# Kernel optimization log

Measured on AMD Instinct MI355X. Metric: run time of the kernel, lower is better.

## Reference

```python
import jax, jax.numpy as jnp
import numpy as np

N_NODES = 50000
N_EDGES = 800000
D_IN, D_HID, D_OUT = 128, 128, 64
BN_EPS = 1e-5


def gcn_conv(x, W, b, src, dst, ew, n):
    # PyG GCNConv: out[i] = sum_j norm_ij * (x @ W)[j] + b, with self-loops added
    xw = x @ W                                   # [N, D_out]
    loop = jnp.arange(n)
    s = jnp.concatenate([src, loop])             # add self-loops (weight 1)
    d = jnp.concatenate([dst, loop])
    w = jnp.concatenate([ew, jnp.ones((n,), x.dtype)])
    deg = jax.ops.segment_sum(w, d, num_segments=n)
    dinv = jnp.where(deg > 0, jax.lax.rsqrt(deg), 0.0)
    norm = dinv[s] * w * dinv[d]                 # symmetric normalization
    msg = xw[s] * norm[:, None]                  # gather + scale  [E+N, D_out]
    return jax.ops.segment_sum(msg, d, num_segments=n) + b


def setup_inputs() -> dict:
    key = jax.random.key(0)
    ks = jax.random.split(key, 12)
    x = jax.random.normal(ks[0], (N_NODES, D_IN), dtype=jnp.float32)
    edge_index = jax.random.randint(ks[1], (2, N_EDGES), 0, N_NODES, dtype=jnp.int64)
    edge_weight = jax.random.uniform(ks[2], (N_EDGES,), dtype=jnp.float32)
    W1 = jax.random.normal(ks[3], (D_IN, D_HID), dtype=jnp.float32) * 0.05
    b1 = jnp.zeros((D_HID,), jnp.float32)
    gamma = jnp.ones((D_HID,), jnp.float32)
    beta = jnp.zeros((D_HID,), jnp.float32)
    running_mean = jax.random.normal(ks[4], (D_HID,), dtype=jnp.float32) * 0.1
    running_var = jax.random.uniform(ks[5], (D_HID,), dtype=jnp.float32) + 0.5
    W2 = jax.random.normal(ks[6], (D_HID, D_OUT), dtype=jnp.float32) * 0.05
    b2 = jnp.zeros((D_OUT,), jnp.float32)
    return {"x": x, "edge_index": edge_index, "edge_weight": edge_weight,
            "W1": W1, "b1": b1, "gamma": gamma, "beta": beta,
            "running_mean": running_mean, "running_var": running_var,
            "W2": W2, "b2": b2}


def reference(x, edge_index, edge_weight, W1, b1, gamma, beta,
              running_mean, running_var, W2, b2):
    src, dst = edge_index[0], edge_index[1]
    n = x.shape[0]
    h = gcn_conv(x, W1, b1, src, dst, edge_weight, n)
    # BatchNorm1d in eval mode (running stats); dropout inactive in eval
    h = (h - running_mean) * jax.lax.rsqrt(running_var + BN_EPS) * gamma + beta
    h = jax.nn.relu(h)
    out = gcn_conv(h, W2, b2, src, dst, edge_weight, n)
    return out
```

## Files before the change

### kernel.cpp

```cpp
#include <hip/hip_runtime.h>
#include <hip/hip_fp16.h>

#define BN_EPS 1e-5f
#define PAD 64

static __device__ __forceinline__ unsigned short f2bf(float f) {
    unsigned u = __float_as_uint(f);
    u += 0x7FFF + ((u >> 16) & 1);
    return (unsigned short)(u >> 16);
}
static __device__ __forceinline__ float bf2f(unsigned short b) {
    return __uint_as_float((unsigned)b << 16);
}
static __device__ __forceinline__ unsigned pk(int s, float w) {
    return ((unsigned)s << 16) | (unsigned)__half_as_ushort(__float2half_rn(w));
}
static __device__ __forceinline__ float pw(unsigned e) {
    return __half2float(__ushort_as_half((unsigned short)(e & 0xFFFFu)));
}

__global__ __launch_bounds__(256) void k_fused(const int* __restrict__ src, const int* __restrict__ dst,
                                               const float* __restrict__ ew,
                                               int* cnt, unsigned* __restrict__ pad, int e, int gfill, int stride,
                                               const float* __restrict__ A, const float* __restrict__ W,
                                               unsigned short* __restrict__ C, int n,
                                               const float* __restrict__ b1, const float* __restrict__ gamma,
                                               const float* __restrict__ beta, const float* __restrict__ mean,
                                               const float* __restrict__ var,
                                               float* __restrict__ bnscale, float* __restrict__ bnshift) {
    __shared__ float WsQ[32 * 128];
    __shared__ float AsT[128 * 32];
    int tid = threadIdx.x;
    int b = (int)blockIdx.x;
    int gGemm = (n + 31) / 32;

    bool isFill = ((b % stride) == 0) && (b / stride < gfill);
    if (isFill) {
        int i0 = ((b / stride) * 256 + tid) * 8;
        if (i0 + 7 < e) {
            int4   s0 = *(const int4*)(src + i0), s1 = *(const int4*)(src + i0 + 4);
            int4   d0 = *(const int4*)(dst + i0), d1 = *(const int4*)(dst + i0 + 4);
            float4 w0 = *(const float4*)(ew + i0), w1 = *(const float4*)(ew + i0 + 4);
            int p0 = atomicAdd(&cnt[d0.x], 1);
            int p1 = atomicAdd(&cnt[d0.y], 1);
            int p2 = atomicAdd(&cnt[d0.z], 1);
            int p3 = atomicAdd(&cnt[d0.w], 1);
            int p4 = atomicAdd(&cnt[d1.x], 1);
            int p5 = atomicAdd(&cnt[d1.y], 1);
            int p6 = atomicAdd(&cnt[d1.z], 1);
            int p7 = atomicAdd(&cnt[d1.w], 1);
            if (p0 < PAD) pad[(size_t)d0.x * PAD + p0] = pk(s0.x, w0.x);
            if (p1 < PAD) pad[(size_t)d0.y * PAD + p1] = pk(s0.y, w0.y);
            if (p2 < PAD) pad[(size_t)d0.z * PAD + p2] = pk(s0.z, w0.z);
            if (p3 < PAD) pad[(size_t)d0.w * PAD + p3] = pk(s0.w, w0.w);
            if (p4 < PAD) pad[(size_t)d1.x * PAD + p4] = pk(s1.x, w1.x);
            if (p5 < PAD) pad[(size_t)d1.y * PAD + p5] = pk(s1.y, w1.y);
            if (p6 < PAD) pad[(size_t)d1.z * PAD + p6] = pk(s1.z, w1.z);
            if (p7 < PAD) pad[(size_t)d1.w * PAD + p7] = pk(s1.w, w1.w);
        } else {
            for (int i = i0; i < e; ++i) {
                int d = dst[i];
                int p = atomicAdd(&cnt[d], 1);
                if (p < PAD) pad[(size_t)d * PAD + p] = pk(src[i], ew[i]);
            }
        }
        return;
    }

    int fillsBefore = (b == 0) ? 0 : min(gfill, (b - 1) / stride + 1);
    int g = b - fillsBefore;
    if (g == gGemm) {
        if (tid < 128) {
            float sc = gamma[tid] * rsqrtf(var[tid] + BN_EPS);
            bnscale[tid] = sc;
            bnshift[tid] = (b1[tid] - mean[tid]) * sc + beta[tid];
        }
        return;
    }

    int row0 = g * 32;
    {
        int lr = tid & 31, kq = tid >> 5;
        int gr = row0 + lr; if (gr > n - 1) gr = n - 1;
        const float4* A4 = (const float4*)(A + (size_t)gr * 128);
        #pragma unroll
        for (int j = 0; j < 4; ++j) {
            float4 v = A4[kq * 4 + j];
            int k = kq * 16 + j * 4;
            AsT[(k + 0) * 32 + lr] = v.x;
            AsT[(k + 1) * 32 + lr] = v.y;
            AsT[(k + 2) * 32 + lr] = v.z;
            AsT[(k + 3) * 32 + lr] = v.w;
        }
    }
    int cg = tid & 31, rg = tid >> 5;
    float4 acc0 = make_float4(0, 0, 0, 0), acc1 = acc0, acc2 = acc0, acc3 = acc0;
    const float4* W4 = (const float4*)W;
    float4* WsQ4 = (float4*)WsQ;
    const float4* AsT4 = (const float4*)AsT;
    for (int ph = 0; ph < 4; ++ph) {
        __syncthreads();
        #pragma unroll
        for (int j = 0; j < 4; ++j)
            WsQ4[j * 256 + tid] = W4[ph * 1024 + j * 256 + tid];
        __syncthreads();
        #pragma unroll 16
        for (int kk = 0; kk < 32; ++kk) {
            float4 w = WsQ4[kk * 32 + cg];
            float4 a = AsT4[(ph * 32 + kk) * 8 + rg];
            acc0.x += a.x * w.x; acc0.y += a.x * w.y; acc0.z += a.x * w.z; acc0.w += a.x * w.w;
            acc1.x += a.y * w.x; acc1.y += a.y * w.y; acc1.z += a.y * w.z; acc1.w += a.y * w.w;
            acc2.x += a.z * w.x; acc2.y += a.z * w.y; acc2.z += a.z * w.z; acc2.w += a.z * w.w;
            acc3.x += a.w * w.x; acc3.y += a.w * w.y; acc3.z += a.w * w.z; acc3.w += a.w * w.w;
        }
    }
    ushort4* C4 = (ushort4*)C;
    int r = row0 + rg * 4;
    if (r + 0 < n) C4[(size_t)(r + 0) * 32 + cg] = make_ushort4(f2bf(acc0.x), f2bf(acc0.y), f2bf(acc0.z), f2bf(acc0.w));
    if (r + 1 < n) C4[(size_t)(r + 1) * 32 + cg] = make_ushort4(f2bf(acc1.x), f2bf(acc1.y), f2bf(acc1.z), f2bf(acc1.w));
    if (r + 2 < n) C4[(size_t)(r + 2) * 32 + cg] = make_ushort4(f2bf(acc2.x), f2bf(acc2.y), f2bf(acc2.z), f2bf(acc2.w));
    if (r + 3 < n) C4[(size_t)(r + 3) * 32 + cg] = make_ushort4(f2bf(acc3.x), f2bf(acc3.y), f2bf(acc3.z), f2bf(acc3.w));
}

__global__ __launch_bounds__(256) void k_deg(const int* __restrict__ cnt, const unsigned* __restrict__ pad,
                                             float* __restrict__ dinv, int n) {
    int i = blockIdx.x * 256 + threadIdx.x;
    if (i < n) {
        int c = min(cnt[i], PAD);
        size_t base = (size_t)i * PAD;
        const uint4* row = (const uint4*)(pad + base);
        float s = 1.0f;
        int p = 0;
        for (; p + 3 < c; p += 4) {
            uint4 v = row[p >> 2];
            s += pw(v.x) + pw(v.y) + pw(v.z) + pw(v.w);
        }
        for (; p < c; ++p) s += pw(pad[base + p]);
        dinv[i] = rsqrtf(s);
    }
}

__global__ __launch_bounds__(256) void k_gemm2(const unsigned short* __restrict__ A, const float* __restrict__ W,
                                               unsigned short* __restrict__ C, int n) {
    __shared__ float Ws[128 * 64];
    __shared__ float AsT[128 * 32];
    int tid = threadIdx.x;
    int row0 = blockIdx.x * 32;
    {
        const float4* W4 = (const float4*)W;
        float4* Ws4 = (float4*)Ws;
        #pragma unroll
        for (int j = 0; j < 8; ++j) Ws4[j * 256 + tid] = W4[j * 256 + tid];
    }
    {
        int lr = tid & 31, kq = tid >> 5;
        int gr = row0 + lr; if (gr > n - 1) gr = n - 1;
        const ushort4* A4 = (const ushort4*)(A + (size_t)gr * 128);
        #pragma unroll
        for (int j = 0; j < 4; ++j) {
            ushort4 v = A4[kq * 4 + j];
            int k = kq * 16 + j * 4;
            AsT[(k + 0) * 32 + lr] = bf2f(v.x);
            AsT[(k + 1) * 32 + lr] = bf2f(v.y);
            AsT[(k + 2) * 32 + lr] = bf2f(v.z);
            AsT[(k + 3) * 32 + lr] = bf2f(v.w);
        }
    }
    __syncthreads();
    int cg = tid & 15;
    int rg = tid >> 4;
    float4 acc0 = make_float4(0, 0, 0, 0), acc1 = acc0;
    const float4* Ws4c = (const float4*)Ws;
    const float2* AsT2 = (const float2*)AsT;
    #pragma unroll 16
    for (int k = 0; k < 128; ++k) {
        float4 w = Ws4c[k * 16 + cg];
        float2 a = AsT2[k * 16 + rg];
        acc0.x += a.x * w.x; acc0.y += a.x * w.y; acc0.z += a.x * w.z; acc0.w += a.x * w.w;
        acc1.x += a.y * w.x; acc1.y += a.y * w.y; acc1.z += a.y * w.z; acc1.w += a.y * w.w;
    }
    ushort4* C4 = (ushort4*)C;
    int r = row0 + rg * 2;
    if (r + 0 < n) C4[(size_t)(r + 0) * 16 + cg] = make_ushort4(f2bf(acc0.x), f2bf(acc0.y), f2bf(acc0.z), f2bf(acc0.w));
    if (r + 1 < n) C4[(size_t)(r + 1) * 16 + cg] = make_ushort4(f2bf(acc1.x), f2bf(acc1.y), f2bf(acc1.z), f2bf(acc1.w));
}

__global__ __launch_bounds__(256) void k_agg1(const unsigned short* __restrict__ xw, const int* __restrict__ cnt,
                                              const unsigned* __restrict__ pad,
                                              const float* __restrict__ dinv,
                                              const float* __restrict__ scale, const float* __restrict__ shift,
                                              unsigned short* __restrict__ h, int n) {
    int node = blockIdx.x * 8 + (threadIdx.x >> 5);
    if (node >= n) return;
    int lc = threadIdx.x & 31;
    const ushort4* X4 = (const ushort4*)xw;
    float di = dinv[node];
    int c = min(cnt[node], PAD);
    size_t base = (size_t)node * PAD;
    ushort4 q0 = X4[(size_t)node * 32 + lc];
    float4 acc0 = make_float4(bf2f(q0.x) * di, bf2f(q0.y) * di, bf2f(q0.z) * di, bf2f(q0.w) * di);
    float4 acc1 = make_float4(0, 0, 0, 0);
    float4 acc2 = make_float4(0, 0, 0, 0);
    float4 acc3 = make_float4(0, 0, 0, 0);
    int p = 0;
    for (; p + 3 < c; p += 4) {
        uint4 ee = *(const uint4*)(pad + base + p);
        float w0 = pw(ee.x) * dinv[ee.x >> 16];
        float w1 = pw(ee.y) * dinv[ee.y >> 16];
        float w2 = pw(ee.z) * dinv[ee.z >> 16];
        float w3 = pw(ee.w) * dinv[ee.w >> 16];
        ushort4 a = X4[(size_t)(ee.x >> 16) * 32 + lc];
        ushort4 b = X4[(size_t)(ee.y >> 16) * 32 + lc];
        ushort4 g = X4[(size_t)(ee.z >> 16) * 32 + lc];
        ushort4 d = X4[(size_t)(ee.w >> 16) * 32 + lc];
        acc0.x += w0 * bf2f(a.x); acc0.y += w0 * bf2f(a.y); acc0.z += w0 * bf2f(a.z); acc0.w += w0 * bf2f(a.w);
        acc1.x += w1 * bf2f(b.x); acc1.y += w1 * bf2f(b.y); acc1.z += w1 * bf2f(b.z); acc1.w += w1 * bf2f(b.w);
        acc2.x += w2 * bf2f(g.x); acc2.y += w2 * bf2f(g.y); acc2.z += w2 * bf2f(g.z); acc2.w += w2 * bf2f(g.w);
        acc3.x += w3 * bf2f(d.x); acc3.y += w3 * bf2f(d.y); acc3.z += w3 * bf2f(d.z); acc3.w += w3 * bf2f(d.w);
    }
    for (; p < c; ++p) {
        unsigned e0 = pad[base + p];
        float w0 = pw(e0) * dinv[e0 >> 16];
        ushort4 a = X4[(size_t)(e0 >> 16) * 32 + lc];
        acc0.x += w0 * bf2f(a.x); acc0.y += w0 * bf2f(a.y); acc0.z += w0 * bf2f(a.z); acc0.w += w0 * bf2f(a.w);
    }
    acc0.x = (acc0.x + acc1.x + acc2.x + acc3.x) * di;
    acc0.y = (acc0.y + acc1.y + acc2.y + acc3.y) * di;
    acc0.z = (acc0.z + acc1.z + acc2.z + acc3.z) * di;
    acc0.w = (acc0.w + acc1.w + acc2.w + acc3.w) * di;
    float4 Sc = ((const float4*)scale)[lc];
    float4 Sh = ((const float4*)shift)[lc];
    ushort4 r;
    r.x = f2bf(fmaxf(acc0.x * Sc.x + Sh.x, 0.0f));
    r.y = f2bf(fmaxf(acc0.y * Sc.y + Sh.y, 0.0f));
    r.z = f2bf(fmaxf(acc0.z * Sc.z + Sh.z, 0.0f));
    r.w = f2bf(fmaxf(acc0.w * Sc.w + Sh.w, 0.0f));
    ((ushort4*)h)[(size_t)node * 32 + lc] = r;
}

__global__ __launch_bounds__(256) void k_agg2(const unsigned short* __restrict__ hw, const int* __restrict__ cnt,
                                              const unsigned* __restrict__ pad,
                                              const float* __restrict__ dinv,
                                              const float* __restrict__ b2, float* __restrict__ out, int n) {
    int node = blockIdx.x * 16 + (threadIdx.x >> 4);
    if (node >= n) return;
    int lc = threadIdx.x & 15;
    const ushort4* X4 = (const ushort4*)hw;
    float di = dinv[node];
    int c = min(cnt[node], PAD);
    size_t base = (size_t)node * PAD;
    ushort4 q0 = X4[(size_t)node * 16 + lc];
    float4 acc0 = make_float4(bf2f(q0.x) * di, bf2f(q0.y) * di, bf2f(q0.z) * di, bf2f(q0.w) * di);
    float4 acc1 = make_float4(0, 0, 0, 0);
    float4 acc2 = make_float4(0, 0, 0, 0);
    float4 acc3 = make_float4(0, 0, 0, 0);
    int p = 0;
    for (; p + 3 < c; p += 4) {
        uint4 ee = *(const uint4*)(pad + base + p);
        float w0 = pw(ee.x) * dinv[ee.x >> 16];
        float w1 = pw(ee.y) * dinv[ee.y >> 16];
        float w2 = pw(ee.z) * dinv[ee.z >> 16];
        float w3 = pw(ee.w) * dinv[ee.w >> 16];
        ushort4 a = X4[(size_t)(ee.x >> 16) * 16 + lc];
        ushort4 b = X4[(size_t)(ee.y >> 16) * 16 + lc];
        ushort4 g = X4[(size_t)(ee.z >> 16) * 16 + lc];
        ushort4 d = X4[(size_t)(ee.w >> 16) * 16 + lc];
        acc0.x += w0 * bf2f(a.x); acc0.y += w0 * bf2f(a.y); acc0.z += w0 * bf2f(a.z); acc0.w += w0 * bf2f(a.w);
        acc1.x += w1 * bf2f(b.x); acc1.y += w1 * bf2f(b.y); acc1.z += w1 * bf2f(b.z); acc1.w += w1 * bf2f(b.w);
        acc2.x += w2 * bf2f(g.x); acc2.y += w2 * bf2f(g.y); acc2.z += w2 * bf2f(g.z); acc2.w += w2 * bf2f(g.w);
        acc3.x += w3 * bf2f(d.x); acc3.y += w3 * bf2f(d.y); acc3.z += w3 * bf2f(d.z); acc3.w += w3 * bf2f(d.w);
    }
    for (; p < c; ++p) {
        unsigned e0 = pad[base + p];
        float w0 = pw(e0) * dinv[e0 >> 16];
        ushort4 a = X4[(size_t)(e0 >> 16) * 16 + lc];
        acc0.x += w0 * bf2f(a.x); acc0.y += w0 * bf2f(a.y); acc0.z += w0 * bf2f(a.z); acc0.w += w0 * bf2f(a.w);
    }
    float4 B = ((const float4*)b2)[lc];
    acc0.x = (acc0.x + acc1.x + acc2.x + acc3.x) * di + B.x;
    acc0.y = (acc0.y + acc1.y + acc2.y + acc3.y) * di + B.y;
    acc0.z = (acc0.z + acc1.z + acc2.z + acc3.z) * di + B.z;
    acc0.w = (acc0.w + acc1.w + acc2.w + acc3.w) * di + B.w;
    ((float4*)out)[(size_t)node * 16 + lc] = acc0;
}


extern "C" void kernel_launch(void* const* d_in, const int* in_sizes, int n_in,
                              void* d_out, int out_size, void* d_ws, size_t ws_size,
                              hipStream_t stream) {
    const float* x     = (const float*)d_in[0];
    const int*   ei    = (const int*)d_in[1];
    const float* ew    = (const float*)d_in[2];
    const float* W1    = (const float*)d_in[3];
    const float* b1    = (const float*)d_in[4];
    const float* gamma = (const float*)d_in[5];
    const float* beta  = (const float*)d_in[6];
    const float* rmean = (const float*)d_in[7];
    const float* rvar  = (const float*)d_in[8];
    const float* W2    = (const float*)d_in[9];
    const float* b2    = (const float*)d_in[10];
    float* out = (float*)d_out;

    int N = in_sizes[0] / 128;
    int E = in_sizes[2];
    const int* src = ei;
    const int* dst = ei + E;

    char* p = (char*)d_ws;
    auto carve = [&](size_t bytes) { char* q = p; p += (bytes + 255) & ~(size_t)255; return (void*)q; };
    int*      cnt     = (int*)     carve(sizeof(int) * (size_t)N);
    unsigned* pad     = (unsigned*)carve(sizeof(unsigned) * (size_t)N * PAD);
    float*    dinv    = (float*)   carve(sizeof(float) * (size_t)N);
    float*    bnscale = (float*)   carve(sizeof(float) * 128);
    float*    bnshift = (float*)   carve(sizeof(float) * 128);
    unsigned short* xw1 = (unsigned short*)carve(sizeof(unsigned short) * (size_t)N * 128);
    unsigned short* h   = (unsigned short*)carve(sizeof(unsigned short) * (size_t)N * 128);
    unsigned short* hw2 = (unsigned short*)carve(sizeof(unsigned short) * (size_t)N * 64);

    int gN    = (N + 255) / 256;
    int gFill = (E + 2047) / 2048;
    int gGemm = (N + 31) / 32;
    int T     = gFill + gGemm + 1;
    int S     = T / gFill;
    if (S < 2) S = 2;

    hipMemsetAsync(cnt, 0, sizeof(int) * (size_t)N, stream);
    k_fused <<<T, 256, 0, stream>>>(src, dst, ew, cnt, pad, E, gFill, S,
                                    x, W1, xw1, N,
                                    b1, gamma, beta, rmean, rvar, bnscale, bnshift);
    k_deg   <<<gN, 256, 0, stream>>>(cnt, pad, dinv, N);
    k_agg1  <<<(N + 7) / 8, 256, 0, stream>>>(xw1, cnt, pad, dinv, bnscale, bnshift, h, N);
    k_gemm2 <<<(N + 31) / 32, 256, 0, stream>>>(h, W2, hw2, N);
    k_agg2  <<<(N + 15) / 16, 256, 0, stream>>>(hw2, cnt, pad, dinv, b2, out, N);
}
```

Measured before the change: 218.7 us.

## Fuse all GCN stages into one cooperative persistent kernel with grid syncs

Replaces the memset plus five separate kernel launches with a single cooperative kernel that runs every stage (count reset, BN params, edge bucketing alongside GEMM1, degree, aggregation 1, GEMM2, aggregation 2) in grid-stride loops separated by grid.sync. The aim is to remove launch gaps and inter-kernel drain. In exchange the grid is capped at 1024 blocks and each stage loops over persistent blocks, which can lower per-stage parallelism and add grid-barrier cost. If the cooperative launch fails, the original multi-kernel path still runs.

Result: slower. 564.8 us (+158.2%).

```diff
diff --git a/kernel.cpp b/kernel.cpp
--- a/kernel.cpp
+++ b/kernel.cpp
@@ -1,5 +1,8 @@
 #include <hip/hip_runtime.h>
 #include <hip/hip_fp16.h>
+#include <hip/hip_cooperative_groups.h>
+
+namespace cg = cooperative_groups;
 
 #define BN_EPS 1e-5f
 #define PAD 64
@@ -18,6 +21,284 @@
 static __device__ __forceinline__ float pw(unsigned e) {
     return __half2float(__ushort_as_half((unsigned short)(e & 0xFFFFu)));
 }
+
+__global__ __launch_bounds__(256, 4) void k_all(
+    const int* __restrict__ src, const int* __restrict__ dst, const float* __restrict__ ew,
+    int* __restrict__ cnt, unsigned* __restrict__ pad, int e,
+    const float* __restrict__ x, const float* __restrict__ W1,
+    unsigned short* __restrict__ xw1, int n,
+    const float* __restrict__ b1, const float* __restrict__ gamma,
+    const float* __restrict__ beta, const float* __restrict__ mean,
+    const float* __restrict__ var,
+    float* __restrict__ bnscale, float* __restrict__ bnshift,
+    float* __restrict__ dinv, const float* __restrict__ W2,
+    unsigned short* __restrict__ h, unsigned short* __restrict__ hw2,
+    const float* __restrict__ b2, float* __restrict__ out)
+{
+    cg::grid_group grid = cg::this_grid();
+    __shared__ float smem[8192];
+    int tid = threadIdx.x;
+    int b   = (int)blockIdx.x;
+    int nb  = (int)gridDim.x;
+
+    for (int i = b * 256 + tid; i < n; i += nb * 256) cnt[i] = 0;
+    if (b == 0 && tid < 128) {
+        float sc = gamma[tid] * rsqrtf(var[tid] + BN_EPS);
+        bnscale[tid] = sc;
+        bnshift[tid] = (b1[tid] - mean[tid]) * sc + beta[tid];
+    }
+    grid.sync();
+
+    int CF    = (e + 2047) / 2048;
+    int gGemm = (n + 31) / 32;
+    if ((b & 3) == 0) {
+        for (int chunk = b >> 2; chunk < CF; chunk += nb >> 2) {
+            int i0 = chunk * 2048 + tid * 8;
+            if (i0 + 7 < e) {
+                int4   s0 = *(const int4*)(src + i0), s1 = *(const int4*)(src + i0 + 4);
+                int4   d0 = *(const int4*)(dst + i0), d1 = *(const int4*)(dst + i0 + 4);
+                float4 w0 = *(const float4*)(ew + i0), w1 = *(const float4*)(ew + i0 + 4);
+                int p0 = atomicAdd(&cnt[d0.x], 1);
+                int p1 = atomicAdd(&cnt[d0.y], 1);
+                int p2 = atomicAdd(&cnt[d0.z], 1);
+                int p3 = atomicAdd(&cnt[d0.w], 1);
+                int p4 = atomicAdd(&cnt[d1.x], 1);
+                int p5 = atomicAdd(&cnt[d1.y], 1);
+                int p6 = atomicAdd(&cnt[d1.z], 1);
+                int p7 = atomicAdd(&cnt[d1.w], 1);
+                if (p0 < PAD) pad[(size_t)d0.x * PAD + p0] = pk(s0.x, w0.x);
+                if (p1 < PAD) pad[(size_t)d0.y * PAD + p1] = pk(s0.y, w0.y);
+                if (p2 < PAD) pad[(size_t)d0.z * PAD + p2] = pk(s0.z, w0.z);
+                if (p3 < PAD) pad[(size_t)d0.w * PAD + p3] = pk(s0.w, w0.w);
+                if (p4 < PAD) pad[(size_t)d1.x * PAD + p4] = pk(s1.x, w1.x);
+                if (p5 < PAD) pad[(size_t)d1.y * PAD + p5] = pk(s1.y, w1.y);
+                if (p6 < PAD) pad[(size_t)d1.z * PAD + p6] = pk(s1.z, w1.z);
+                if (p7 < PAD) pad[(size_t)d1.w * PAD + p7] = pk(s1.w, w1.w);
+            } else {
+                for (int i = i0; i < e; ++i) {
+                    int d = dst[i];
+                    int p = atomicAdd(&cnt[d], 1);
+                    if (p < PAD) pad[(size_t)d * PAD + p] = pk(src[i], ew[i]);
+                }
+            }
+        }
+    } else {
+        int j  = b - (b >> 2) - 1;
+        int js = nb - (nb >> 2);
+        float* WsQ = smem;
+        float* AsT = smem + 4096;
+        float4* WsQ4 = (float4*)WsQ;
+        const float4* AsT4 = (const float4*)AsT;
+        const float4* W4 = (const float4*)W1;
+        for (int t = j; t < gGemm; t += js) {
+            int row0 = t * 32;
+            {
+                int lr = tid & 31, kq = tid >> 5;
+                int gr = row0 + lr; if (gr > n - 1) gr = n - 1;
+                const float4* A4 = (const float4*)(x + (size_t)gr * 128);
+                #pragma unroll
+                for (int q = 0; q < 4; ++q) {
+                    float4 v = A4[kq * 4 + q];
+                    int k = kq * 16 + q * 4;
+                    AsT[(k + 0) * 32 + lr] = v.x;
+                    AsT[(k + 1) * 32 + lr] = v.y;
+                    AsT[(k + 2) * 32 + lr] = v.z;
+                    AsT[(k + 3) * 32 + lr] = v.w;
+                }
+            }
+            int cg_ = tid & 31, rg = tid >> 5;
+            float4 acc0 = make_float4(0, 0, 0, 0), acc1 = acc0, acc2 = acc0, acc3 = acc0;
+            for (int ph = 0; ph < 4; ++ph) {
+                __syncthreads();
+                #pragma unroll
+                for (int q = 0; q < 4; ++q)
+                    WsQ4[q * 256 + tid] = W4[ph * 1024 + q * 256 + tid];
+                __syncthreads();
+                #pragma unroll 16
+                for (int kk = 0; kk < 32; ++kk) {
+                    float4 w = WsQ4[kk * 32 + cg_];
+                    float4 a = AsT4[(ph * 32 + kk) * 8 + rg];
+                    acc0.x += a.x * w.x; acc0.y += a.x * w.y; acc0.z += a.x * w.z; acc0.w += a.x * w.w;
+                    acc1.x += a.y * w.x; acc1.y += a.y * w.y; acc1.z += a.y * w.z; acc1.w += a.y * w.w;
+                    acc2.x += a.z * w.x; acc2.y += a.z * w.y; acc2.z += a.z * w.z; acc2.w += a.z * w.w;
+                    acc3.x += a.w * w.x; acc3.y += a.w * w.y; acc3.z += a.w * w.z; acc3.w += a.w * w.w;
+                }
+            }
+            __syncthreads();
+            ushort4* C4 = (ushort4*)xw1;
+            int r = row0 + rg * 4;
+            if (r + 0 < n) C4[(size_t)(r + 0) * 32 + cg_] = make_ushort4(f2bf(acc0.x), f2bf(acc0.y), f2bf(acc0.z), f2bf(acc0.w));
+            if (r + 1 < n) C4[(size_t)(r + 1) * 32 + cg_] = make_ushort4(f2bf(acc1.x), f2bf(acc1.y), f2bf(acc1.z), f2bf(acc1.w));
+            if (r + 2 < n) C4[(size_t)(r + 2) * 32 + cg_] = make_ushort4(f2bf(acc2.x), f2bf(acc2.y), f2bf(acc2.z), f2bf(acc2.w));
+            if (r + 3 < n) C4[(size_t)(r + 3) * 32 + cg_] = make_ushort4(f2bf(acc3.x), f2bf(acc3.y), f2bf(acc3.z), f2bf(acc3.w));
+        }
+    }
+    grid.sync();
+
+    for (int i = b * 256 + tid; i < n; i += nb * 256) {
+        int c = min(cnt[i], PAD);
+        size_t base = (size_t)i * PAD;
+        const uint4* row = (const uint4*)(pad + base);
+        float s = 1.0f;
+        int p = 0;
+        for (; p + 3 < c; p += 4) {
+            uint4 v = row[p >> 2];
+            s += pw(v.x) + pw(v.y) + pw(v.z) + pw(v.w);
+        }
+        for (; p < c; ++p) s += pw(pad[base + p]);
+        dinv[i] = rsqrtf(s);
+    }
+    grid.sync();
+
+    {
+        int ngrp = (n + 7) / 8;
+        const ushort4* X4 = (const ushort4*)xw1;
+        for (int vb = b; vb < ngrp; vb += nb) {
+            int node = vb * 8 + (tid >> 5);
+            if (node < n) {
+                int lc = tid & 31;
+                float di = dinv[node];
+                int c = min(cnt[node], PAD);
+                size_t base = (size_t)node * PAD;
+                ushort4 q0 = X4[(size_t)node * 32 + lc];
+                float4 acc0 = make_float4(bf2f(q0.x) * di, bf2f(q0.y) * di, bf2f(q0.z) * di, bf2f(q0.w) * di);
+                float4 acc1 = make_float4(0, 0, 0, 0);
+                float4 acc2 = make_float4(0, 0, 0, 0);
+                float4 acc3 = make_float4(0, 0, 0, 0);
+                int p = 0;
+                for (; p + 3 < c; p += 4) {
+                    uint4 ee = *(const uint4*)(pad + base + p);
+                    float w0 = pw(ee.x) * dinv[ee.x >> 16];
+                    float w1 = pw(ee.y) * dinv[ee.y >> 16];
+                    float w2 = pw(ee.z) * dinv[ee.z >> 16];
+                    float w3 = pw(ee.w) * dinv[ee.w >> 16];
+                    ushort4 a = X4[(size_t)(ee.x >> 16) * 32 + lc];
+                    ushort4 bb = X4[(size_t)(ee.y >> 16) * 32 + lc];
+                    ushort4 g = X4[(size_t)(ee.z >> 16) * 32 + lc];
+                    ushort4 d = X4[(size_t)(ee.w >> 16) * 32 + lc];
+                    acc0.x += w0 * bf2f(a.x); acc0.y += w0 * bf2f(a.y); acc0.z += w0 * bf2f(a.z); acc0.w += w0 * bf2f(a.w);
+                    acc1.x += w1 * bf2f(bb.x); acc1.y += w1 * bf2f(bb.y); acc1.z += w1 * bf2f(bb.z); acc1.w += w1 * bf2f(bb.w);
+                    acc2.x += w2 * bf2f(g.x); acc2.y += w2 * bf2f(g.y); acc2.z += w2 * bf2f(g.z); acc2.w += w2 * bf2f(g.w);
+                    acc3.x += w3 * bf2f(d.x); acc3.y += w3 * bf2f(d.y); acc3.z += w3 * bf2f(d.z); acc3.w += w3 * bf2f(d.w);
+                }
+                for (; p < c; ++p) {
+                    unsigned e0 = pad[base + p];
+                    float w0 = pw(e0) * dinv[e0 >> 16];
+                    ushort4 a = X4[(size_t)(e0 >> 16) * 32 + lc];
+                    acc0.x += w0 * bf2f(a.x); acc0.y += w0 * bf2f(a.y); acc0.z += w0 * bf2f(a.z); acc0.w += w0 * bf2f(a.w);
+                }
+                acc0.x = (acc0.x + acc1.x + acc2.x + acc3.x) * di;
+                acc0.y = (acc0.y + acc1.y + acc2.y + acc3.y) * di;
+                acc0.z = (acc0.z + acc1.z + acc2.z + acc3.z) * di;
+                acc0.w = (acc0.w + acc1.w + acc2.w + acc3.w) * di;
+                float4 Sc = ((const float4*)bnscale)[lc];
+                float4 Sh = ((const float4*)bnshift)[lc];
+                ushort4 r;
+                r.x = f2bf(fmaxf(acc0.x * Sc.x + Sh.x, 0.0f));
+                r.y = f2bf(fmaxf(acc0.y * Sc.y + Sh.y, 0.0f));
+                r.z = f2bf(fmaxf(acc0.z * Sc.z + Sh.z, 0.0f));
+                r.w = f2bf(fmaxf(acc0.w * Sc.w + Sh.w, 0.0f));
+                ((ushort4*)h)[(size_t)node * 32 + lc] = r;
+            }
+        }
+    }
+    grid.sync();
+
+    {
+        float* WsQ = smem;
+        float* AsT = smem + 4096;
+        float4* WsQ4 = (float4*)WsQ;
+        const float2* AsT2 = (const float2*)AsT;
+        const float4* W4 = (const float4*)W2;
+        for (int t = b; t < gGemm; t += nb) {
+            int row0 = t * 32;
+            {
+                int lr = tid & 31, kq = tid >> 5;
+                int gr = row0 + lr; if (gr > n - 1) gr = n - 1;
+                const ushort4* A4 = (const ushort4*)(h + (size_t)gr * 128);
+                #pragma unroll
+                for (int q = 0; q < 4; ++q) {
+                    ushort4 v = A4[kq * 4 + q];
+                    int k = kq * 16 + q * 4;
+                    AsT[(k + 0) * 32 + lr] = bf2f(v.x);
+                    AsT[(k + 1) * 32 + lr] = bf2f(v.y);
+                    AsT[(k + 2) * 32 + lr] = bf2f(v.z);
+                    AsT[(k + 3) * 32 + lr] = bf2f(v.w);
+                }
+            }
+            int cg_ = tid & 15, rg = tid >> 4;
+            float4 acc0 = make_float4(0, 0, 0, 0), acc1 = acc0;
+            for (int ph = 0; ph < 4; ++ph) {
+                __syncthreads();
+                #pragma unroll
+                for (int q = 0; q < 2; ++q)
+                    WsQ4[q * 256 + tid] = W4[ph * 512 + q * 256 + tid];
+                __syncthreads();
+                #pragma unroll 16
+                for (int kk = 0; kk < 32; ++kk) {
+                    float4 w = WsQ4[kk * 16 + cg_];
+                    float2 a = AsT2[(ph * 32 + kk) * 16 + rg];
+                    acc0.x += a.x * w.x; acc0.y += a.x * w.y; acc0.z += a.x * w.z; acc0.w += a.x * w.w;
+                    acc1.x += a.y * w.x; acc1.y += a.y * w.y; acc1.z += a.y * w.z; acc1.w += a.y * w.w;
+                }
+            }
+            __syncthreads();
+            ushort4* C4 = (ushort4*)hw2;
+            int r = row0 + rg * 2;
+            if (r + 0 < n) C4[(size_t)(r + 0) * 16 + cg_] = make_ushort4(f2bf(acc0.x), f2bf(acc0.y), f2bf(acc0.z), f2bf(acc0.w));
+            if (r + 1 < n) C4[(size_t)(r + 1) * 16 + cg_] = make_ushort4(f2bf(acc1.x), f2bf(acc1.y), f2bf(acc1.z), f2bf(acc1.w));
+        }
+    }
+    grid.sync();
+
+    {
+        int ngrp = (n + 15) / 16;
+        const ushort4* X4 = (const ushort4*)hw2;
+        for (int vb = b; vb < ngrp; vb += nb) {
+            int node = vb * 16 + (tid >> 4);
+            if (node < n) {
+                int lc = tid & 15;
+                float di = dinv[node];
+                int c = min(cnt[node], PAD);
+                size_t base = (size_t)node * PAD;
+                ushort4 q0 = X4[(size_t)node * 16 + lc];
+                float4 acc0 = make_float4(bf2f(q0.x) * di, bf2f(q0.y) * di, bf2f(q0.z) * di, bf2f(q0.w) * di);
+                float4 acc1 = make_float4(0, 0, 0, 0);
+                float4 acc2 = make_float4(0, 0, 0, 0);
+                float4 acc3 = make_float4(0, 0, 0, 0);
+                int p = 0;
+                for (; p + 3 < c; p += 4) {
+                    uint4 ee = *(const uint4*)(pad + base + p);
+                    float w0 = pw(ee.x) * dinv[ee.x >> 16];
+                    float w1 = pw(ee.y) * dinv[ee.y >> 16];
+                    float w2 = pw(ee.z) * dinv[ee.z >> 16];
+                    float w3 = pw(ee.w) * dinv[ee.w >> 16];
+                    ushort4 a = X4[(size_t)(ee.x >> 16) * 16 + lc];
+                    ushort4 bb = X4[(size_t)(ee.y >> 16) * 16 + lc];
+                    ushort4 g = X4[(size_t)(ee.z >> 16) * 16 + lc];
+                    ushort4 d = X4[(size_t)(ee.w >> 16) * 16 + lc];
+                    acc0.x += w0 * bf2f(a.x); acc0.y += w0 * bf2f(a.y); acc0.z += w0 * bf2f(a.z); acc0.w += w0 * bf2f(a.w);
+                    acc1.x += w1 * bf2f(bb.x); acc1.y += w1 * bf2f(bb.y); acc1.z += w1 * bf2f(bb.z); acc1.w += w1 * bf2f(bb.w);
+                    acc2.x += w2 * bf2f(g.x); acc2.y += w2 * bf2f(g.y); acc2.z += w2 * bf2f(g.z); acc2.w += w2 * bf2f(g.w);
+                    acc3.x += w3 * bf2f(d.x); acc3.y += w3 * bf2f(d.y); acc3.z += w3 * bf2f(d.z); acc3.w += w3 * bf2f(d.w);
+                }
+                for (; p < c; ++p) {
+                    unsigned e0 = pad[base + p];
+                    float w0 = pw(e0) * dinv[e0 >> 16];
+                    ushort4 a = X4[(size_t)(e0 >> 16) * 16 + lc];
+                    acc0.x += w0 * bf2f(a.x); acc0.y += w0 * bf2f(a.y); acc0.z += w0 * bf2f(a.z); acc0.w += w0 * bf2f(a.w);
+                }
+                float4 B = ((const float4*)b2)[lc];
+                acc0.x = (acc0.x + acc1.x + acc2.x + acc3.x) * di + B.x;
+                acc0.y = (acc0.y + acc1.y + acc2.y + acc3.y) * di + B.y;
+                acc0.z = (acc0.z + acc1.z + acc2.z + acc3.z) * di + B.z;
+                acc0.w = (acc0.w + acc1.w + acc2.w + acc3.w) * di + B.w;
+                ((float4*)out)[(size_t)node * 16 + lc] = acc0;
+            }
+        }
+    }
+}
+
 
 __global__ __launch_bounds__(256) void k_fused(const int* __restrict__ src, const int* __restrict__ dst,
                                                const float* __restrict__ ew,
@@ -93,7 +374,7 @@
             AsT[(k + 3) * 32 + lr] = v.w;
         }
     }
-    int cg = tid & 31, rg = tid >> 5;
+    int cg_ = tid & 31, rg = tid >> 5;
     float4 acc0 = make_float4(0, 0, 0, 0), acc1 = acc0, acc2 = acc0, acc3 = acc0;
     const float4* W4 = (const float4*)W;
     float4* WsQ4 = (float4*)WsQ;
@@ -106,7 +387,7 @@
         __syncthreads();
         #pragma unroll 16
         for (int kk = 0; kk < 32; ++kk) {
-            float4 w = WsQ4[kk * 32 + cg];
+            float4 w = WsQ4[kk * 32 + cg_];
             float4 a = AsT4[(ph * 32 + kk) * 8 + rg];
             acc0.x += a.x * w.x; acc0.y += a.x * w.y; acc0.z += a.x * w.z; acc0.w += a.x * w.w;
             acc1.x += a.y * w.x; acc1.y += a.y * w.y; acc1.z += a.y * w.z; acc1.w += a.y * w.w;
@@ -116,10 +397,10 @@
     }
     ushort4* C4 = (ushort4*)C;
     int r = row0 + rg * 4;
-    if (r + 0 < n) C4[(size_t)(r + 0) * 32 + cg] = make_ushort4(f2bf(acc0.x), f2bf(acc0.y), f2bf(acc0.z), f2bf(acc0.w));
-    if (r + 1 < n) C4[(size_t)(r + 1) * 32 + cg] = make_ushort4(f2bf(acc1.x), f2bf(acc1.y), f2bf(acc1.z), f2bf(acc1.w));
-    if (r + 2 < n) C4[(size_t)(r + 2) * 32 + cg] = make_ushort4(f2bf(acc2.x), f2bf(acc2.y), f2bf(acc2.z), f2bf(acc2.w));
-    if (r + 3 < n) C4[(size_t)(r + 3) * 32 + cg] = make_ushort4(f2bf(acc3.x), f2bf(acc3.y), f2bf(acc3.z), f2bf(acc3.w));
+    if (r + 0 < n) C4[(size_t)(r + 0) * 32 + cg_] = make_ushort4(f2bf(acc0.x), f2bf(acc0.y), f2bf(acc0.z), f2bf(acc0.w));
+    if (r + 1 < n) C4[(size_t)(r + 1) * 32 + cg_] = make_ushort4(f2bf(acc1.x), f2bf(acc1.y), f2bf(acc1.z), f2bf(acc1.w));
+    if (r + 2 < n) C4[(size_t)(r + 2) * 32 + cg_] = make_ushort4(f2bf(acc2.x), f2bf(acc2.y), f2bf(acc2.z), f2bf(acc2.w));
+    if (r + 3 < n) C4[(size_t)(r + 3) * 32 + cg_] = make_ushort4(f2bf(acc3.x), f2bf(acc3.y), f2bf(acc3.z), f2bf(acc3.w));
 }
 
 __global__ __launch_bounds__(256) void k_deg(const int* __restrict__ cnt, const unsigned* __restrict__ pad,
@@ -167,22 +448,22 @@
         }
     }
     __syncthreads();
-    int cg = tid & 15;
+    int cg_ = tid & 15;
     int rg = tid >> 4;
     float4 acc0 = make_float4(0, 0, 0, 0), acc1 = acc0;
     const float4* Ws4c = (const float4*)Ws;
     const float2* AsT2 = (const float2*)AsT;
     #pragma unroll 16
     for (int k = 0; k < 128; ++k) {
-        float4 w = Ws4c[k * 16 + cg];
+        float4 w = Ws4c[k * 16 + cg_];
         float2 a = AsT2[k * 16 + rg];
         acc0.x += a.x * w.x; acc0.y += a.x * w.y; acc0.z += a.x * w.z; acc0.w += a.x * w.w;
         acc1.x += a.y * w.x; acc1.y += a.y * w.y; acc1.z += a.y * w.z; acc1.w += a.y * w.w;
     }
     ushort4* C4 = (ushort4*)C;
     int r = row0 + rg * 2;
-    if (r + 0 < n) C4[(size_t)(r + 0) * 16 + cg] = make_ushort4(f2bf(acc0.x), f2bf(acc0.y), f2bf(acc0.z), f2bf(acc0.w));
-    if (r + 1 < n) C4[(size_t)(r + 1) * 16 + cg] = make_ushort4(f2bf(acc1.x), f2bf(acc1.y), f2bf(acc1.z), f2bf(acc1.w));
+    if (r + 0 < n) C4[(size_t)(r + 0) * 16 + cg_] = make_ushort4(f2bf(acc0.x), f2bf(acc0.y), f2bf(acc0.z), f2bf(acc0.w));
+    if (r + 1 < n) C4[(size_t)(r + 1) * 16 + cg_] = make_ushort4(f2bf(acc1.x), f2bf(acc1.y), f2bf(acc1.z), f2bf(acc1.w));
 }
 
 __global__ __launch_bounds__(256) void k_agg1(const unsigned short* __restrict__ xw, const int* __restrict__ cnt,
@@ -317,6 +598,29 @@
     unsigned short* h   = (unsigned short*)carve(sizeof(unsigned short) * (size_t)N * 128);
     unsigned short* hw2 = (unsigned short*)carve(sizeof(unsigned short) * (size_t)N * 64);
 
+    int maxBperCU = 0;
+    hipError_t qerr = hipOccupancyMaxActiveBlocksPerMultiprocessor(&maxBperCU, (const void*)k_all, 256, 0);
+    hipError_t cerr = hipErrorUnknown;
+    if (qerr == hipSuccess && maxBperCU > 0) {
+        int grid = maxBperCU * 256;
+        if (grid > 1024) grid = 1024;
+        grid &= ~3;
+        if (grid >= 8) {
+            void* args[] = {
+                (void*)&src, (void*)&dst, (void*)&ew,
+                (void*)&cnt, (void*)&pad, (void*)&E,
+                (void*)&x, (void*)&W1, (void*)&xw1, (void*)&N,
+                (void*)&b1, (void*)&gamma, (void*)&beta, (void*)&rmean, (void*)&rvar,
+                (void*)&bnscale, (void*)&bnshift,
+                (void*)&dinv, (void*)&W2,
+                (void*)&h, (void*)&hw2,
+                (void*)&b2, (void*)&out
+            };
+            cerr = hipLaunchCooperativeKernel((const void*)k_all, dim3(grid), dim3(256), args, 0, stream);
+        }
+    }
+    if (cerr == hipSuccess) return;
+
     int gN    = (N + 255) / 256;
     int gFill = (E + 2047) / 2048;
     int gGemm = (N + 31) / 32;
```

## Fuse second-layer GEMM into first aggregation kernel via shared-memory W2

Applied to the files above, without the earlier changes.

Merges the layer-1 aggregation (with BN+ReLU) and the layer-2 dense transform into one kernel. Each block aggregates 8 nodes, stores their hidden rows in shared memory, and multiplies by a bf16 copy of W2 staged in shared memory. This removes the intermediate h buffer round trip and one launch. In exchange, every block reloads and converts W2, which uses more shared memory and may lower occupancy, and W2 is rounded to bf16.

New measurement: 219.5 us. About the same (+0.4%).

```diff
diff --git a/kernel.cpp b/kernel.cpp
--- a/kernel.cpp
+++ b/kernel.cpp
@@ -93,7 +93,7 @@
             AsT[(k + 3) * 32 + lr] = v.w;
         }
     }
-    int cg = tid & 31, rg = tid >> 5;
+    int cg_ = tid & 31, rg = tid >> 5;
     float4 acc0 = make_float4(0, 0, 0, 0), acc1 = acc0, acc2 = acc0, acc3 = acc0;
     const float4* W4 = (const float4*)W;
     float4* WsQ4 = (float4*)WsQ;
@@ -106,7 +106,7 @@
         __syncthreads();
         #pragma unroll 16
         for (int kk = 0; kk < 32; ++kk) {
-            float4 w = WsQ4[kk * 32 + cg];
+            float4 w = WsQ4[kk * 32 + cg_];
             float4 a = AsT4[(ph * 32 + kk) * 8 + rg];
             acc0.x += a.x * w.x; acc0.y += a.x * w.y; acc0.z += a.x * w.z; acc0.w += a.x * w.w;
             acc1.x += a.y * w.x; acc1.y += a.y * w.y; acc1.z += a.y * w.z; acc1.w += a.y * w.w;
@@ -116,10 +116,10 @@
     }
     ushort4* C4 = (ushort4*)C;
     int r = row0 + rg * 4;
-    if (r + 0 < n) C4[(size_t)(r + 0) * 32 + cg] = make_ushort4(f2bf(acc0.x), f2bf(acc0.y), f2bf(acc0.z), f2bf(acc0.w));
-    if (r + 1 < n) C4[(size_t)(r + 1) * 32 + cg] = make_ushort4(f2bf(acc1.x), f2bf(acc1.y), f2bf(acc1.z), f2bf(acc1.w));
-    if (r + 2 < n) C4[(size_t)(r + 2) * 32 + cg] = make_ushort4(f2bf(acc2.x), f2bf(acc2.y), f2bf(acc2.z), f2bf(acc2.w));
-    if (r + 3 < n) C4[(size_t)(r + 3) * 32 + cg] = make_ushort4(f2bf(acc3.x), f2bf(acc3.y), f2bf(acc3.z), f2bf(acc3.w));
+    if (r + 0 < n) C4[(size_t)(r + 0) * 32 + cg_] = make_ushort4(f2bf(acc0.x), f2bf(acc0.y), f2bf(acc0.z), f2bf(acc0.w));
+    if (r + 1 < n) C4[(size_t)(r + 1) * 32 + cg_] = make_ushort4(f2bf(acc1.x), f2bf(acc1.y), f2bf(acc1.z), f2bf(acc1.w));
+    if (r + 2 < n) C4[(size_t)(r + 2) * 32 + cg_] = make_ushort4(f2bf(acc2.x), f2bf(acc2.y), f2bf(acc2.z), f2bf(acc2.w));
+    if (r + 3 < n) C4[(size_t)(r + 3) * 32 + cg_] = make_ushort4(f2bf(acc3.x), f2bf(acc3.y), f2bf(acc3.z), f2bf(acc3.w));
 }
 
 __global__ __launch_bounds__(256) void k_deg(const int* __restrict__ cnt, const unsigned* __restrict__ pad,
@@ -140,102 +140,91 @@
     }
 }
 
-__global__ __launch_bounds__(256) void k_gemm2(const unsigned short* __restrict__ A, const float* __restrict__ W,
-                                               unsigned short* __restrict__ C, int n) {
-    __shared__ float Ws[128 * 64];
-    __shared__ float AsT[128 * 32];
-    int tid = threadIdx.x;
-    int row0 = blockIdx.x * 32;
-    {
-        const float4* W4 = (const float4*)W;
-        float4* Ws4 = (float4*)Ws;
-        #pragma unroll
-        for (int j = 0; j < 8; ++j) Ws4[j * 256 + tid] = W4[j * 256 + tid];
-    }
-    {
-        int lr = tid & 31, kq = tid >> 5;
-        int gr = row0 + lr; if (gr > n - 1) gr = n - 1;
-        const ushort4* A4 = (const ushort4*)(A + (size_t)gr * 128);
-        #pragma unroll
-        for (int j = 0; j < 4; ++j) {
-            ushort4 v = A4[kq * 4 + j];
-            int k = kq * 16 + j * 4;
-            AsT[(k + 0) * 32 + lr] = bf2f(v.x);
-            AsT[(k + 1) * 32 + lr] = bf2f(v.y);
-            AsT[(k + 2) * 32 + lr] = bf2f(v.z);
-            AsT[(k + 3) * 32 + lr] = bf2f(v.w);
-        }
-    }
-    __syncthreads();
-    int cg = tid & 15;
-    int rg = tid >> 4;
-    float4 acc0 = make_float4(0, 0, 0, 0), acc1 = acc0;
-    const float4* Ws4c = (const float4*)Ws;
-    const float2* AsT2 = (const float2*)AsT;
-    #pragma unroll 16
-    for (int k = 0; k < 128; ++k) {
-        float4 w = Ws4c[k * 16 + cg];
-        float2 a = AsT2[k * 16 + rg];
-        acc0.x += a.x * w.x; acc0.y += a.x * w.y; acc0.z += a.x * w.z; acc0.w += a.x * w.w;
-        acc1.x += a.y * w.x; acc1.y += a.y * w.y; acc1.z += a.y * w.z; acc1.w += a.y * w.w;
-    }
-    ushort4* C4 = (ushort4*)C;
-    int r = row0 + rg * 2;
-    if (r + 0 < n) C4[(size_t)(r + 0) * 16 + cg] = make_ushort4(f2bf(acc0.x), f2bf(acc0.y), f2bf(acc0.z), f2bf(acc0.w));
-    if (r + 1 < n) C4[(size_t)(r + 1) * 16 + cg] = make_ushort4(f2bf(acc1.x), f2bf(acc1.y), f2bf(acc1.z), f2bf(acc1.w));
-}
-
-__global__ __launch_bounds__(256) void k_agg1(const unsigned short* __restrict__ xw, const int* __restrict__ cnt,
+__global__ __launch_bounds__(256) void k_ag12(const unsigned short* __restrict__ xw, const int* __restrict__ cnt,
                                               const unsigned* __restrict__ pad,
                                               const float* __restrict__ dinv,
                                               const float* __restrict__ scale, const float* __restrict__ shift,
-                                              unsigned short* __restrict__ h, int n) {
-    int node = blockIdx.x * 8 + (threadIdx.x >> 5);
-    if (node >= n) return;
-    int lc = threadIdx.x & 31;
-    const ushort4* X4 = (const ushort4*)xw;
-    float di = dinv[node];
-    int c = min(cnt[node], PAD);
-    size_t base = (size_t)node * PAD;
-    ushort4 q0 = X4[(size_t)node * 32 + lc];
-    float4 acc0 = make_float4(bf2f(q0.x) * di, bf2f(q0.y) * di, bf2f(q0.z) * di, bf2f(q0.w) * di);
-    float4 acc1 = make_float4(0, 0, 0, 0);
-    float4 acc2 = make_float4(0, 0, 0, 0);
-    float4 acc3 = make_float4(0, 0, 0, 0);
-    int p = 0;
-    for (; p + 3 < c; p += 4) {
-        uint4 ee = *(const uint4*)(pad + base + p);
-        float w0 = pw(ee.x) * dinv[ee.x >> 16];
-        float w1 = pw(ee.y) * dinv[ee.y >> 16];
-        float w2 = pw(ee.z) * dinv[ee.z >> 16];
-        float w3 = pw(ee.w) * dinv[ee.w >> 16];
-        ushort4 a = X4[(size_t)(ee.x >> 16) * 32 + lc];
-        ushort4 b = X4[(size_t)(ee.y >> 16) * 32 + lc];
-        ushort4 g = X4[(size_t)(ee.z >> 16) * 32 + lc];
-        ushort4 d = X4[(size_t)(ee.w >> 16) * 32 + lc];
-        acc0.x += w0 * bf2f(a.x); acc0.y += w0 * bf2f(a.y); acc0.z += w0 * bf2f(a.z); acc0.w += w0 * bf2f(a.w);
-        acc1.x += w1 * bf2f(b.x); acc1.y += w1 * bf2f(b.y); acc1.z += w1 * bf2f(b.z); acc1.w += w1 * bf2f(b.w);
-        acc2.x += w2 * bf2f(g.x); acc2.y += w2 * bf2f(g.y); acc2.z += w2 * bf2f(g.z); acc2.w += w2 * bf2f(g.w);
-        acc3.x += w3 * bf2f(d.x); acc3.y += w3 * bf2f(d.y); acc3.z += w3 * bf2f(d.z); acc3.w += w3 * bf2f(d.w);
-    }
-    for (; p < c; ++p) {
-        unsigned e0 = pad[base + p];
-        float w0 = pw(e0) * dinv[e0 >> 16];
-        ushort4 a = X4[(size_t)(e0 >> 16) * 32 + lc];
-        acc0.x += w0 * bf2f(a.x); acc0.y += w0 * bf2f(a.y); acc0.z += w0 * bf2f(a.z); acc0.w += w0 * bf2f(a.w);
-    }
-    acc0.x = (acc0.x + acc1.x + acc2.x + acc3.x) * di;
-    acc0.y = (acc0.y + acc1.y + acc2.y + acc3.y) * di;
-    acc0.z = (acc0.z + acc1.z + acc2.z + acc3.z) * di;
-    acc0.w = (acc0.w + acc1.w + acc2.w + acc3.w) * di;
-    float4 Sc = ((const float4*)scale)[lc];
-    float4 Sh = ((const float4*)shift)[lc];
-    ushort4 r;
-    r.x = f2bf(fmaxf(acc0.x * Sc.x + Sh.x, 0.0f));
-    r.y = f2bf(fmaxf(acc0.y * Sc.y + Sh.y, 0.0f));
-    r.z = f2bf(fmaxf(acc0.z * Sc.z + Sh.z, 0.0f));
-    r.w = f2bf(fmaxf(acc0.w * Sc.w + Sh.w, 0.0f));
-    ((ushort4*)h)[(size_t)node * 32 + lc] = r;
+                                              const float* __restrict__ W2,
+                                              unsigned short* __restrict__ hw2, int n) {
+    __shared__ unsigned short W2s[128 * 64];
+    __shared__ unsigned short hs[8 * 128];
+    int tid = threadIdx.x;
+    {
+        const float4* W4 = (const float4*)W2;
+        #pragma unroll
+        for (int q = 0; q < 8; ++q) {
+            float4 v = W4[q * 256 + tid];
+            ((ushort4*)W2s)[q * 256 + tid] = make_ushort4(f2bf(v.x), f2bf(v.y), f2bf(v.z), f2bf(v.w));
+        }
+    }
+    int g = tid >> 5;
+    int lc = tid & 31;
+    int node = blockIdx.x * 8 + g;
+    if (node < n) {
+        const ushort4* X4 = (const ushort4*)xw;
+        float di = dinv[node];
+        int c = min(cnt[node], PAD);
+        size_t base = (size_t)node * PAD;
+        ushort4 q0 = X4[(size_t)node * 32 + lc];
+        float4 acc0 = make_float4(bf2f(q0.x) * di, bf2f(q0.y) * di, bf2f(q0.z) * di, bf2f(q0.w) * di);
+        float4 acc1 = make_float4(0, 0, 0, 0);
+        float4 acc2 = make_float4(0, 0, 0, 0);
+        float4 acc3 = make_float4(0, 0, 0, 0);
+        int p = 0;
+        for (; p + 3 < c; p += 4) {
+            uint4 ee = *(const uint4*)(pad + base + p);
+            float w0 = pw(ee.x) * dinv[ee.x >> 16];
+            float w1 = pw(ee.y) * dinv[ee.y >> 16];
+            float w2 = pw(ee.z) * dinv[ee.z >> 16];
+            float w3 = pw(ee.w) * dinv[ee.w >> 16];
+            ushort4 a = X4[(size_t)(ee.x >> 16) * 32 + lc];
+            ushort4 b = X4[(size_t)(ee.y >> 16) * 32 + lc];
+            ushort4 gg = X4[(size_t)(ee.z >> 16) * 32 + lc];
+            ushort4 d = X4[(size_t)(ee.w >> 16) * 32 + lc];
+            acc0.x += w0 * bf2f(a.x); acc0.y += w0 * bf2f(a.y); acc0.z += w0 * bf2f(a.z); acc0.w += w0 * bf2f(a.w);
+            acc1.x += w1 * bf2f(b.x); acc1.y += w1 * bf2f(b.y); acc1.z += w1 * bf2f(b.z); acc1.w += w1 * bf2f(b.w);
+            acc2.x += w2 * bf2f(gg.x); acc2.y += w2 * bf2f(gg.y); acc2.z += w2 * bf2f(gg.z); acc2.w += w2 * bf2f(gg.w);
+            acc3.x += w3 * bf2f(d.x); acc3.y += w3 * bf2f(d.y); acc3.z += w3 * bf2f(d.z); acc3.w += w3 * bf2f(d.w);
+        }
+        for (; p < c; ++p) {
+            unsigned e0 = pad[base + p];
+            float w0 = pw(e0) * dinv[e0 >> 16];
+            ushort4 a = X4[(size_t)(e0 >> 16) * 32 + lc];
+            acc0.x += w0 * bf2f(a.x); acc0.y += w0 * bf2f(a.y); acc0.z += w0 * bf2f(a.z); acc0.w += w0 * bf2f(a.w);
+        }
+        acc0.x = (acc0.x + acc1.x + acc2.x + acc3.x) * di;
+        acc0.y = (acc0.y + acc1.y + acc2.y + acc3.y) * di;
+        acc0.z = (acc0.z + acc1.z + acc2.z + acc3.z) * di;
+        acc0.w = (acc0.w + acc1.w + acc2.w + acc3.w) * di;
+        float4 Sc = ((const float4*)scale)[lc];
+        float4 Sh = ((const float4*)shift)[lc];
+        ushort4 r;
+        r.x = f2bf(fmaxf(acc0.x * Sc.x + Sh.x, 0.0f));
+        r.y = f2bf(fmaxf(acc0.y * Sc.y + Sh.y, 0.0f));
+        r.z = f2bf(fmaxf(acc0.z * Sc.z + Sh.z, 0.0f));
+        r.w = f2bf(fmaxf(acc0.w * Sc.w + Sh.w, 0.0f));
+        ((ushort4*)hs)[g * 32 + lc] = r;
+    }
+    __syncthreads();
+    if (node < n) {
+        float a0 = 0.0f, a1 = 0.0f;
+        const unsigned* W2u = (const unsigned*)W2s;
+        const unsigned* hu  = (const unsigned*)(hs + g * 128);
+        #pragma unroll 8
+        for (int k2 = 0; k2 < 64; ++k2) {
+            unsigned hp = hu[k2];
+            float h0 = bf2f((unsigned short)(hp & 0xFFFFu));
+            float h1 = bf2f((unsigned short)(hp >> 16));
+            unsigned w0u = W2u[(2 * k2) * 32 + lc];
+            unsigned w1u = W2u[(2 * k2 + 1) * 32 + lc];
+            a0 += h0 * bf2f((unsigned short)(w0u & 0xFFFFu));
+            a1 += h0 * bf2f((unsigned short)(w0u >> 16));
+            a0 += h1 * bf2f((unsigned short)(w1u & 0xFFFFu));
+            a1 += h1 * bf2f((unsigned short)(w1u >> 16));
+        }
+        unsigned outp = ((unsigned)f2bf(a1) << 16) | (unsigned)f2bf(a0);
+        ((unsigned*)hw2)[(size_t)node * 32 + lc] = outp;
+    }
 }
 
 __global__ __launch_bounds__(256) void k_agg2(const unsigned short* __restrict__ hw, const int* __restrict__ cnt,
@@ -314,7 +303,6 @@
     float*    bnscale = (float*)   carve(sizeof(float) * 128);
     float*    bnshift = (float*)   carve(sizeof(float) * 128);
     unsigned short* xw1 = (unsigned short*)carve(sizeof(unsigned short) * (size_t)N * 128);
-    unsigned short* h   = (unsigned short*)carve(sizeof(unsigned short) * (size_t)N * 128);
     unsigned short* hw2 = (unsigned short*)carve(sizeof(unsigned short) * (size_t)N * 64);
 
     int gN    = (N + 255) / 256;
@@ -329,7 +317,6 @@
                                     x, W1, xw1, N,
                                     b1, gamma, beta, rmean, rvar, bnscale, bnshift);
     k_deg   <<<gN, 256, 0, stream>>>(cnt, pad, dinv, N);
-    k_agg1  <<<(N + 7) / 8, 256, 0, stream>>>(xw1, cnt, pad, dinv, bnscale, bnshift, h, N);
-    k_gemm2 <<<(N + 31) / 32, 256, 0, stream>>>(h, W2, hw2, N);
+    k_ag12  <<<(N + 7) / 8, 256, 0, stream>>>(xw1, cnt, pad, dinv, bnscale, bnshift, W2, hw2, N);
     k_agg2  <<<(N + 15) / 16, 256, 0, stream>>>(hw2, cnt, pad, dinv, b2, out, N);
 }
```
